# Performance work log

Measured on AMD Instinct MI355X. Metric: run time of the kernel, lower is better.

## Reference

```python
import jax, jax.numpy as jnp
import numpy as np

FP8_MAX = 448.0  # max finite value of float8_e4m3fn
F8 = jnp.float8_e4m3fn


def setup_inputs() -> dict:
    key = jax.random.key(0)
    kx, kw, kb = jax.random.split(key, 3)
    B, S, K, N = 4, 2048, 4096, 16384
    x = jax.random.normal(kx, (B, S, K), dtype=jnp.float32)
    # Pre-quantized symmetric per-tensor FP8 weight: simulate quantization of a
    # realistically initialized fp32 weight with scale ws.
    ws = jnp.float32(0.01)
    w_fp32 = jax.random.normal(kw, (N, K), dtype=jnp.float32) * 0.02
    weight = jnp.clip(w_fp32 / ws, -FP8_MAX, FP8_MAX).astype(F8)  # [N, K] fp8
    weight_scale = jnp.full((1,), ws, dtype=jnp.float32)  # per-tensor strategy
    bias = jax.random.normal(kb, (N,), dtype=jnp.float32) * 0.01
    return {"x": x, "weight": weight, "weight_scale": weight_scale, "bias": bias}


def reference(x, weight, weight_scale, bias):
    # Dynamic per-tensor fp8 quantization of the activation (torchao
    # _input_activation_quant_func_fp8 with PerTensor granularity):
    # (input_scale * weight_scale), plus bias.
    amax = jnp.max(jnp.abs(x))
    x_scale = jnp.maximum(amax, jnp.float32(1e-12)) / FP8_MAX
    xq = jnp.clip(x / x_scale, -FP8_MAX, FP8_MAX).astype(F8).astype(jnp.float32)
    w = weight.astype(jnp.float32)  # [N, K]
    out = jnp.einsum("bsk,nk->bsn", xq, w)  # [B, S, N]
    out = out * (x_scale * weight_scale[0]) + bias
    return out
```

## Files before the change

### kernel.cpp

```cpp
#include <hip/hip_runtime.h>
#include <hip/hip_fp8.h>
#include <hip/hip_fp16.h>
#include <stdint.h>

#define FP8_MAX_V 448.0f

typedef float f32x16 __attribute__((ext_vector_type(16)));
typedef int i32x4 __attribute__((ext_vector_type(4)));
typedef int i32x8 __attribute__((ext_vector_type(8)));

__device__ __forceinline__ uint8_t cvt_fp8(float v) {
    return __hip_cvt_float_to_fp8(fminf(fmaxf(v, -FP8_MAX_V), FP8_MAX_V),
                                  __HIP_SATFINITE, __HIP_E4M3);
}

__global__ void fp8lin_probe(const uint32_t* __restrict__ w, unsigned* __restrict__ flag,
                             unsigned* __restrict__ amax_bits) {
    __shared__ unsigned s32, s16, s4;
    if (threadIdx.x == 0) { s32 = 0u; s16 = 0u; s4 = 0u; *amax_bits = 0u; }
    __syncthreads();
    unsigned o32 = 0u, o16 = 0u, o4 = 0u;
    for (int i = threadIdx.x; i < 4096; i += 256) {
        uint32_t v = w[i];
        o32 |= v & 0x000FFFFFu;
        uint32_t h0 = v & 0xFFFFu, h1 = v >> 16;
        o16 |= (h0 & 0x7Fu) | (h1 & 0x7Fu);
        o4  |= (h0 & 0x0Fu) | (h1 & 0x0Fu);
    }
    atomicOr(&s32, o32); atomicOr(&s16, o16); atomicOr(&s4, o4);
    __syncthreads();
    if (threadIdx.x == 0)
        *flag = (s32 == 0u) ? 0u : (s16 == 0u) ? 1u : (s4 == 0u) ? 2u : 3u;
}

__global__ void fp8lin_amax(const float4* __restrict__ x, unsigned* __restrict__ amax_bits, long n4) {
    float m = 0.f;
    long stride = (long)gridDim.x * blockDim.x;
    for (long i = blockIdx.x * (long)blockDim.x + threadIdx.x; i < n4; i += stride) {
        float4 v = x[i];
        m = fmaxf(m, fmaxf(fmaxf(fabsf(v.x), fabsf(v.y)), fmaxf(fabsf(v.z), fabsf(v.w))));
    }
#pragma unroll
    for (int o = 32; o; o >>= 1) m = fmaxf(m, __shfl_xor(m, o));
    if ((threadIdx.x & 63) == 0) atomicMax(amax_bits, __float_as_uint(m));
}

__global__ void fp8lin_quant(const float4* __restrict__ x, const unsigned* __restrict__ amax_bits,
                             uchar4* __restrict__ xq, long n4) {
    float s = fmaxf(__uint_as_float(*amax_bits), 1e-12f) / FP8_MAX_V;
    long stride = (long)gridDim.x * blockDim.x;
    for (long i = blockIdx.x * (long)blockDim.x + threadIdx.x; i < n4; i += stride) {
        float4 v = x[i];
        uchar4 o;
        o.x = cvt_fp8(v.x / s); o.y = cvt_fp8(v.y / s);
        o.z = cvt_fp8(v.z / s); o.w = cvt_fp8(v.w / s);
        xq[i] = o;
    }
}

__global__ void fp8lin_packw(const void* __restrict__ wsrc, const unsigned* __restrict__ flag,
                             uint8_t* __restrict__ pack, int N, int K) {
    const int NKT = K >> 6;
    const long units = ((long)N * K) >> 6;
    unsigned f = *flag;
    long stride = (long)gridDim.x * blockDim.x;
    for (long u = blockIdx.x * (long)blockDim.x + threadIdx.x; u < units; u += stride) {
        int r = (int)(u & 31);
        long v = u >> 5;
        long row = (v / NKT) * 32 + r;
        long kbase = (long)(v % NKT) * 64;
        uint32_t wv[16];
        if (f == 0u) {
            const float4* s = (const float4*)((const float*)wsrc + row * K + kbase);
#pragma unroll
            for (int i = 0; i < 16; ++i) {
                float4 t = s[i];
                wv[i] = (uint32_t)cvt_fp8(t.x) | ((uint32_t)cvt_fp8(t.y) << 8) |
                        ((uint32_t)cvt_fp8(t.z) << 16) | ((uint32_t)cvt_fp8(t.w) << 24);
            }
        } else if (f == 1u) {
            const __half* s = (const __half*)wsrc + row * K + kbase;
#pragma unroll
            for (int i = 0; i < 16; ++i) {
                uint32_t a = 0;
#pragma unroll
                for (int j = 0; j < 4; ++j) a |= (uint32_t)cvt_fp8(__half2float(s[4 * i + j])) << (8 * j);
                wv[i] = a;
            }
        } else if (f == 2u) {
            const uint16_t* s = (const uint16_t*)wsrc + row * K + kbase;
#pragma unroll
            for (int i = 0; i < 16; ++i) {
                uint32_t a = 0;
#pragma unroll
                for (int j = 0; j < 4; ++j)
                    a |= (uint32_t)cvt_fp8(__uint_as_float((uint32_t)s[4 * i + j] << 16)) << (8 * j);
                wv[i] = a;
            }
        } else {
            const uint32_t* s = (const uint32_t*)((const uint8_t*)wsrc + row * K + kbase);
#pragma unroll
            for (int i = 0; i < 16; ++i) wv[i] = s[i];
        }
        uint8_t* d0 = pack + (v * 64 + r) * 32;
        uint8_t* d1 = pack + (v * 64 + 32 + r) * 32;
        i32x4 lo0 = { (int)wv[0], (int)wv[1], (int)wv[2], (int)wv[3] };
        i32x4 lo1 = { (int)wv[4], (int)wv[5], (int)wv[6], (int)wv[7] };
        i32x4 hi0 = { (int)wv[8], (int)wv[9], (int)wv[10], (int)wv[11] };
        i32x4 hi1 = { (int)wv[12], (int)wv[13], (int)wv[14], (int)wv[15] };
        *(i32x4*)(d0) = lo0; *(i32x4*)(d0 + 16) = lo1;
        *(i32x4*)(d1) = hi0; *(i32x4*)(d1 + 16) = hi1;
    }
}

#define BM 128
#define BN 128
#define BK 64
#define A_TILE 8192
#define BUF_BYTES A_TILE
#define SMEM_BYTES (2 * A_TILE)

__device__ __forceinline__ void gload16(const uint8_t* src, uint8_t* ldst) {
    __builtin_amdgcn_global_load_lds(
        (const __attribute__((address_space(1))) uint32_t*)(uintptr_t)src,
        (__attribute__((address_space(3))) uint32_t*)(uintptr_t)ldst, 16, 0, 0);
}

#define WAITVM(N) asm volatile("s_waitcnt vmcnt(" #N ")" ::: "memory")
#define BARRIER() do { asm volatile("" ::: "memory"); __builtin_amdgcn_s_barrier(); \
                       asm volatile("" ::: "memory"); } while (0)

#define LDFRAG(dst, base, off) do {                                    \
    i32x4 _lo = *(const i32x4*)((base) + (off));                       \
    i32x4 _hi = *(const i32x4*)((base) + ((off) ^ 16));                \
    dst[0] = _lo[0]; dst[1] = _lo[1]; dst[2] = _lo[2]; dst[3] = _lo[3];\
    dst[4] = _hi[0]; dst[5] = _hi[1]; dst[6] = _hi[2]; dst[7] = _hi[3];\
} while (0)

#define LOADB(bv, src, koff) do {                                      \
    const uint8_t* _p = (src) + (koff);                                \
    i32x4 _l0 = *(const i32x4*)(_p);                                   \
    i32x4 _l1 = *(const i32x4*)(_p + 16);                               \
    bv[0] = _l0[0]; bv[1] = _l0[1]; bv[2] = _l0[2]; bv[3] = _l0[3];    \
    bv[4] = _l1[0]; bv[5] = _l1[1]; bv[6] = _l1[2]; bv[7] = _l1[3];    \
} while (0)

#define MFMA_MX(A, B, C) __builtin_amdgcn_mfma_scale_f32_32x32x64_f8f6f4( \
    (A), (B), (C), 0, 0, 0, (int)0x7f7f7f7f, 0, (int)0x7f7f7f7f)

__global__ __launch_bounds__(256, 3) void fp8lin_gemm(
    const uint8_t* __restrict__ Aq,
    const uint8_t* __restrict__ Bpack,
    const unsigned* __restrict__ amax_bits,
    const float* __restrict__ wscale,
    const float* __restrict__ bias,
    float* __restrict__ out,
    int M, int N, int K) {
    extern __shared__ __align__(16) uint8_t smem[];

    const int tid = threadIdx.x;
    const int wid = tid >> 6;
    const int lane = tid & 63;
    const int wm = wid >> 1;
    const int wn = wid & 1;

    const int nbx = gridDim.x;
    const int orig = blockIdx.y * nbx + blockIdx.x;
    const int cpx = (gridDim.x * gridDim.y) >> 3;
    const int swzb = (orig & 7) * cpx + (orig >> 3);
    const int brow = (swzb / nbx) * BM;
    const int bcol = (swzb % nbx) * BN;

    const int c0 = tid, c1 = tid + 256;
    const int r0 = c0 >> 2, r1 = c1 >> 2;
    const int sc0 = ((c0 & 3) ^ ((r0 >> 1) & 3)) * 16;
    const int sc1 = ((c1 & 3) ^ ((r1 >> 1) & 3)) * 16;
    const uint8_t* srcA0 = Aq + (size_t)(brow + r0) * K + sc0;
    const uint8_t* srcA1 = Aq + (size_t)(brow + r1) * K + sc1;
    const int ldsW = wid * 1024;

    const int l31 = lane & 31;
    const int q = lane >> 5;
    const int swzr = (l31 >> 1) & 3;
    const int posl = (2 * q) ^ swzr;
    const int offA = (wm * 64 + l31) * 64 + posl * 16;

    const int NKT = K >> 6;
    const uint8_t* srcB0 = Bpack + ((size_t)((bcol >> 5) + wn * 2) * NKT * 64 + lane) * 32;
    const uint8_t* srcB1 = srcB0 + (size_t)NKT * 2048;

    f32x16 acc[2][2];
#pragma unroll
    for (int mi = 0; mi < 2; ++mi)
#pragma unroll
        for (int ni = 0; ni < 2; ++ni)
#pragma unroll
            for (int r = 0; r < 16; ++r) acc[mi][ni][r] = 0.0f;

    auto STAGEA = [&](int t, int ib) {
        size_t k0 = (size_t)t * BK;
        uint8_t* base = smem + ib * BUF_BYTES;
        gload16(srcA0 + k0, base + ldsW);
        gload16(srcA1 + k0, base + ldsW + 4096);
    };

    auto COMPUTE = [&](int ib, const i32x8& b0, const i32x8& b1) {
        const uint8_t* bA = smem + ib * BUF_BYTES;
        i32x8 aX, aY;
        LDFRAG(aX, bA, offA);
        LDFRAG(aY, bA, offA + 2048);
        __builtin_amdgcn_s_setprio(1);
        acc[0][0] = MFMA_MX(aX, b0, acc[0][0]);
        acc[1][0] = MFMA_MX(aY, b0, acc[1][0]);
        acc[0][1] = MFMA_MX(aX, b1, acc[0][1]);
        acc[1][1] = MFMA_MX(aY, b1, acc[1][1]);
        __builtin_amdgcn_s_setprio(0);
    };

    const int NT = K / BK;
    i32x8 bE0, bE1, bO0, bO1;
    LOADB(bE0, srcB0, 0); LOADB(bE1, srcB1, 0);
    STAGEA(0, 0);
    for (int tp = 0; tp < NT; tp += 2) {
        LOADB(bO0, srcB0, (size_t)(tp + 1) * 2048);
        LOADB(bO1, srcB1, (size_t)(tp + 1) * 2048);
        STAGEA(tp + 1, 1);
        WAITVM(6);
        BARRIER();
        COMPUTE(0, bE0, bE1);
        BARRIER();
        if (tp + 2 < NT) {
            LOADB(bE0, srcB0, (size_t)(tp + 2) * 2048);
            LOADB(bE1, srcB1, (size_t)(tp + 2) * 2048);
            STAGEA(tp + 2, 0);
            WAITVM(6);
        } else {
            WAITVM(0);
        }
        BARRIER();
        COMPUTE(1, bO0, bO1);
        BARRIER();
    }

    float s = (fmaxf(__uint_as_float(*amax_bits), 1e-12f) / FP8_MAX_V) * wscale[0];
    const int colg = bcol + wn * 64 + l31;
    const int rowg0 = brow + wm * 64 + 4 * q;
#pragma unroll
    for (int ni = 0; ni < 2; ++ni) {
        int col = colg + ni * 32;
        float bv = bias[col];
#pragma unroll
        for (int mi = 0; mi < 2; ++mi) {
            int rb = rowg0 + mi * 32;
#pragma unroll
            for (int reg = 0; reg < 16; ++reg) {
                int row = rb + (reg & 3) + 8 * (reg >> 2);
                __builtin_nontemporal_store(acc[mi][ni][reg] * s + bv,
                                            out + (size_t)row * N + col);
            }
        }
    }
}

extern "C" void kernel_launch(void* const* d_in, const int* in_sizes, int n_in,
                              void* d_out, int out_size, void* d_ws, size_t ws_size,
                              hipStream_t stream) {
    const float* x = (const float*)d_in[0];
    const void* w = d_in[1];
    const float* wscale = (const float*)d_in[2];
    const float* bias = (const float*)d_in[3];
    float* out = (float*)d_out;

    const int Bb = 4, S = 2048, K = 4096, N = 16384;
    const int M = Bb * S;
    const long nx = (long)M * K;

    unsigned* amax_bits = (unsigned*)d_ws;
    unsigned* wflag = (unsigned*)((char*)d_ws + 32);
    uchar4* xq = (uchar4*)((char*)d_ws + 256);
    uint8_t* pack = (uint8_t*)((char*)d_ws + 256 + nx);

    fp8lin_probe<<<1, 256, 0, stream>>>((const uint32_t*)w, wflag, amax_bits);
    fp8lin_amax<<<2048, 256, 0, stream>>>((const float4*)x, amax_bits, nx / 4);
    fp8lin_quant<<<2048, 256, 0, stream>>>((const float4*)x, amax_bits, xq, nx / 4);
    fp8lin_packw<<<2048, 256, 0, stream>>>(w, wflag, pack, N, K);

    dim3 grid(N / BN, M / BM);
    fp8lin_gemm<<<grid, 256, SMEM_BYTES, stream>>>((const uint8_t*)xq, pack,
                                                   amax_bits, wscale, bias, out, M, N, K);
}
```

Measured before the change: 945.3 us.

## Pre-pack activations into MFMA fragment layout and drop LDS staging in GEMM

The quantize kernel now writes FP8 activations directly in the per-lane MFMA fragment order, mirroring the weight packing, so the GEMM loads A fragments straight from global memory into registers. LDS double-buffering, barriers and the swizzle logic are removed, and the block tile grows to 256 rows with 4x2 accumulators per wave. Occupancy is reduced to 2 blocks per CU. Without LDS sharing, each wave fetches its own A and B fragments from global/L2, and the simple single-iteration prefetch may expose load latency.

```diff
diff --git a/kernel.cpp b/kernel.cpp
--- a/kernel.cpp
+++ b/kernel.cpp
@@ -45,16 +45,24 @@
     if ((threadIdx.x & 63) == 0) atomicMax(amax_bits, __float_as_uint(m));
 }
 
-__global__ void fp8lin_quant(const float4* __restrict__ x, const unsigned* __restrict__ amax_bits,
-                             uchar4* __restrict__ xq, long n4) {
+__global__ void fp8lin_quantpack(const float* __restrict__ x, const unsigned* __restrict__ amax_bits,
+                                 uchar4* __restrict__ apack, int M, int K) {
     float s = fmaxf(__uint_as_float(*amax_bits), 1e-12f) / FP8_MAX_V;
+    const int NKT = K >> 6;
+    const long units = ((long)M * K) >> 2;
     long stride = (long)gridDim.x * blockDim.x;
-    for (long i = blockIdx.x * (long)blockDim.x + threadIdx.x; i < n4; i += stride) {
-        float4 v = x[i];
+    for (long u = blockIdx.x * (long)blockDim.x + threadIdx.x; u < units; u += stride) {
+        long b2 = u & 7;
+        long r = (u >> 3) & 31;
+        long q = (u >> 8) & 1;
+        long v = u >> 9;
+        long row = (v / NKT) * 32 + r;
+        long k = (v % NKT) * 64 + q * 32 + b2 * 4;
+        float4 t = *(const float4*)(x + row * (long)K + k);
         uchar4 o;
-        o.x = cvt_fp8(v.x / s); o.y = cvt_fp8(v.y / s);
-        o.z = cvt_fp8(v.z / s); o.w = cvt_fp8(v.w / s);
-        xq[i] = o;
+        o.x = cvt_fp8(t.x / s); o.y = cvt_fp8(t.y / s);
+        o.z = cvt_fp8(t.z / s); o.w = cvt_fp8(t.w / s);
+        apack[u] = o;
     }
 }
 
@@ -113,34 +121,14 @@
     }
 }
 
-#define BM 128
+#define BM 256
 #define BN 128
 #define BK 64
-#define A_TILE 8192
-#define BUF_BYTES A_TILE
-#define SMEM_BYTES (2 * A_TILE)
-
-__device__ __forceinline__ void gload16(const uint8_t* src, uint8_t* ldst) {
-    __builtin_amdgcn_global_load_lds(
-        (const __attribute__((address_space(1))) uint32_t*)(uintptr_t)src,
-        (__attribute__((address_space(3))) uint32_t*)(uintptr_t)ldst, 16, 0, 0);
-}
-
-#define WAITVM(N) asm volatile("s_waitcnt vmcnt(" #N ")" ::: "memory")
-#define BARRIER() do { asm volatile("" ::: "memory"); __builtin_amdgcn_s_barrier(); \
-                       asm volatile("" ::: "memory"); } while (0)
-
-#define LDFRAG(dst, base, off) do {                                    \
-    i32x4 _lo = *(const i32x4*)((base) + (off));                       \
-    i32x4 _hi = *(const i32x4*)((base) + ((off) ^ 16));                \
-    dst[0] = _lo[0]; dst[1] = _lo[1]; dst[2] = _lo[2]; dst[3] = _lo[3];\
-    dst[4] = _hi[0]; dst[5] = _hi[1]; dst[6] = _hi[2]; dst[7] = _hi[3];\
-} while (0)
-
-#define LOADB(bv, src, koff) do {                                      \
+
+#define LOADF(bv, src, koff) do {                                      \
     const uint8_t* _p = (src) + (koff);                                \
     i32x4 _l0 = *(const i32x4*)(_p);                                   \
-    i32x4 _l1 = *(const i32x4*)(_p + 16);                               \
+    i32x4 _l1 = *(const i32x4*)(_p + 16);                              \
     bv[0] = _l0[0]; bv[1] = _l0[1]; bv[2] = _l0[2]; bv[3] = _l0[3];    \
     bv[4] = _l1[0]; bv[5] = _l1[1]; bv[6] = _l1[2]; bv[7] = _l1[3];    \
 } while (0)
@@ -148,16 +136,14 @@
 #define MFMA_MX(A, B, C) __builtin_amdgcn_mfma_scale_f32_32x32x64_f8f6f4( \
     (A), (B), (C), 0, 0, 0, (int)0x7f7f7f7f, 0, (int)0x7f7f7f7f)
 
-__global__ __launch_bounds__(256, 3) void fp8lin_gemm(
-    const uint8_t* __restrict__ Aq,
+__global__ __launch_bounds__(256, 2) void fp8lin_gemm(
+    const uint8_t* __restrict__ Apack,
     const uint8_t* __restrict__ Bpack,
     const unsigned* __restrict__ amax_bits,
     const float* __restrict__ wscale,
     const float* __restrict__ bias,
     float* __restrict__ out,
     int M, int N, int K) {
-    extern __shared__ __align__(16) uint8_t smem[];
-
     const int tid = threadIdx.x;
     const int wid = tid >> 6;
     const int lane = tid & 63;
@@ -171,86 +157,60 @@
     const int brow = (swzb / nbx) * BM;
     const int bcol = (swzb % nbx) * BN;
 
-    const int c0 = tid, c1 = tid + 256;
-    const int r0 = c0 >> 2, r1 = c1 >> 2;
-    const int sc0 = ((c0 & 3) ^ ((r0 >> 1) & 3)) * 16;
-    const int sc1 = ((c1 & 3) ^ ((r1 >> 1) & 3)) * 16;
-    const uint8_t* srcA0 = Aq + (size_t)(brow + r0) * K + sc0;
-    const uint8_t* srcA1 = Aq + (size_t)(brow + r1) * K + sc1;
-    const int ldsW = wid * 1024;
-
+    const int NKT = K >> 6;
+    const int mt0 = (brow >> 5) + wm * 4;
+    const uint8_t* pA0 = Apack + ((size_t)(mt0 + 0) * NKT * 64 + lane) * 32;
+    const uint8_t* pA1 = Apack + ((size_t)(mt0 + 1) * NKT * 64 + lane) * 32;
+    const uint8_t* pA2 = Apack + ((size_t)(mt0 + 2) * NKT * 64 + lane) * 32;
+    const uint8_t* pA3 = Apack + ((size_t)(mt0 + 3) * NKT * 64 + lane) * 32;
+    const uint8_t* pB0 = Bpack + ((size_t)((bcol >> 5) + wn * 2) * NKT * 64 + lane) * 32;
+    const uint8_t* pB1 = pB0 + (size_t)NKT * 2048;
+
+    f32x16 acc[4][2];
+#pragma unroll
+    for (int mi = 0; mi < 4; ++mi)
+#pragma unroll
+        for (int ni = 0; ni < 2; ++ni)
+#pragma unroll
+            for (int r = 0; r < 16; ++r) acc[mi][ni][r] = 0.0f;
+
+    i32x8 a0, a1, a2, a3, b0, b1;
+    LOADF(a0, pA0, 0); LOADF(a1, pA1, 0);
+    LOADF(a2, pA2, 0); LOADF(a3, pA3, 0);
+    LOADF(b0, pB0, 0); LOADF(b1, pB1, 0);
+
+    const int NT = K / BK;
+#pragma unroll 1
+    for (int t = 0; t < NT; ++t) {
+        __builtin_amdgcn_s_setprio(1);
+        acc[0][0] = MFMA_MX(a0, b0, acc[0][0]);
+        acc[1][0] = MFMA_MX(a1, b0, acc[1][0]);
+        acc[2][0] = MFMA_MX(a2, b0, acc[2][0]);
+        acc[3][0] = MFMA_MX(a3, b0, acc[3][0]);
+        acc[0][1] = MFMA_MX(a0, b1, acc[0][1]);
+        acc[1][1] = MFMA_MX(a1, b1, acc[1][1]);
+        acc[2][1] = MFMA_MX(a2, b1, acc[2][1]);
+        acc[3][1] = MFMA_MX(a3, b1, acc[3][1]);
+        __builtin_amdgcn_s_setprio(0);
+        if (t + 1 < NT) {
+            size_t off = (size_t)(t + 1) * 2048;
+            LOADF(a0, pA0, off); LOADF(a1, pA1, off);
+            LOADF(a2, pA2, off); LOADF(a3, pA3, off);
+            LOADF(b0, pB0, off); LOADF(b1, pB1, off);
+        }
+    }
+
+    float s = (fmaxf(__uint_as_float(*amax_bits), 1e-12f) / FP8_MAX_V) * wscale[0];
     const int l31 = lane & 31;
     const int q = lane >> 5;
-    const int swzr = (l31 >> 1) & 3;
-    const int posl = (2 * q) ^ swzr;
-    const int offA = (wm * 64 + l31) * 64 + posl * 16;
-
-    const int NKT = K >> 6;
-    const uint8_t* srcB0 = Bpack + ((size_t)((bcol >> 5) + wn * 2) * NKT * 64 + lane) * 32;
-    const uint8_t* srcB1 = srcB0 + (size_t)NKT * 2048;
-
-    f32x16 acc[2][2];
-#pragma unroll
-    for (int mi = 0; mi < 2; ++mi)
-#pragma unroll
-        for (int ni = 0; ni < 2; ++ni)
-#pragma unroll
-            for (int r = 0; r < 16; ++r) acc[mi][ni][r] = 0.0f;
-
-    auto STAGEA = [&](int t, int ib) {
-        size_t k0 = (size_t)t * BK;
-        uint8_t* base = smem + ib * BUF_BYTES;
-        gload16(srcA0 + k0, base + ldsW);
-        gload16(srcA1 + k0, base + ldsW + 4096);
-    };
-
-    auto COMPUTE = [&](int ib, const i32x8& b0, const i32x8& b1) {
-        const uint8_t* bA = smem + ib * BUF_BYTES;
-        i32x8 aX, aY;
-        LDFRAG(aX, bA, offA);
-        LDFRAG(aY, bA, offA + 2048);
-        __builtin_amdgcn_s_setprio(1);
-        acc[0][0] = MFMA_MX(aX, b0, acc[0][0]);
-        acc[1][0] = MFMA_MX(aY, b0, acc[1][0]);
-        acc[0][1] = MFMA_MX(aX, b1, acc[0][1]);
-        acc[1][1] = MFMA_MX(aY, b1, acc[1][1]);
-        __builtin_amdgcn_s_setprio(0);
-    };
-
-    const int NT = K / BK;
-    i32x8 bE0, bE1, bO0, bO1;
-    LOADB(bE0, srcB0, 0); LOADB(bE1, srcB1, 0);
-    STAGEA(0, 0);
-    for (int tp = 0; tp < NT; tp += 2) {
-        LOADB(bO0, srcB0, (size_t)(tp + 1) * 2048);
-        LOADB(bO1, srcB1, (size_t)(tp + 1) * 2048);
-        STAGEA(tp + 1, 1);
-        WAITVM(6);
-        BARRIER();
-        COMPUTE(0, bE0, bE1);
-        BARRIER();
-        if (tp + 2 < NT) {
-            LOADB(bE0, srcB0, (size_t)(tp + 2) * 2048);
-            LOADB(bE1, srcB1, (size_t)(tp + 2) * 2048);
-            STAGEA(tp + 2, 0);
-            WAITVM(6);
-        } else {
-            WAITVM(0);
-        }
-        BARRIER();
-        COMPUTE(1, bO0, bO1);
-        BARRIER();
-    }
-
-    float s = (fmaxf(__uint_as_float(*amax_bits), 1e-12f) / FP8_MAX_V) * wscale[0];
     const int colg = bcol + wn * 64 + l31;
-    const int rowg0 = brow + wm * 64 + 4 * q;
+    const int rowg0 = brow + wm * 128 + 4 * q;
 #pragma unroll
     for (int ni = 0; ni < 2; ++ni) {
         int col = colg + ni * 32;
         float bv = bias[col];
 #pragma unroll
-        for (int mi = 0; mi < 2; ++mi) {
+        for (int mi = 0; mi < 4; ++mi) {
             int rb = rowg0 + mi * 32;
 #pragma unroll
             for (int reg = 0; reg < 16; ++reg) {
@@ -277,15 +237,14 @@
 
     unsigned* amax_bits = (unsigned*)d_ws;
     unsigned* wflag = (unsigned*)((char*)d_ws + 32);
-    uchar4* xq = (uchar4*)((char*)d_ws + 256);
-    uint8_t* pack = (uint8_t*)((char*)d_ws + 256 + nx);
+    uint8_t* apack = (uint8_t*)((char*)d_ws + 256);
+    uint8_t* bpack = (uint8_t*)((char*)d_ws + 256 + nx);
 
     fp8lin_probe<<<1, 256, 0, stream>>>((const uint32_t*)w, wflag, amax_bits);
     fp8lin_amax<<<2048, 256, 0, stream>>>((const float4*)x, amax_bits, nx / 4);
-    fp8lin_quant<<<2048, 256, 0, stream>>>((const float4*)x, amax_bits, xq, nx / 4);
-    fp8lin_packw<<<2048, 256, 0, stream>>>(w, wflag, pack, N, K);
+    fp8lin_quantpack<<<2048, 256, 0, stream>>>(x, amax_bits, (uchar4*)apack, M, K);
+    fp8lin_packw<<<2048, 256, 0, stream>>>(w, wflag, bpack, N, K);
 
     dim3 grid(N / BN, M / BM);
-    fp8lin_gemm<<<grid, 256, SMEM_BYTES, stream>>>((const uint8_t*)xq, pack,
-                                                   amax_bits, wscale, bias, out, M, N, K);
-}
+    fp8lin_gemm<<<grid, 256, 0, stream>>>(apack, bpack, amax_bits, wscale, bias, out, M, N, K);
+}
```

New measurement: 820.6 us. -13.2%, faster.
